# Performance work log

Hardware: AMD Instinct MI355X
Metric: run time of the kernel (lower is better)

Reference implementation:

```python
import jax, jax.numpy as jnp
import numpy as np

N_EMBD = 64
HEAD_SIZE = 64
BLOCK_SIZE = 256

def setup_inputs() -> dict:
    key = jax.random.key(0)
    ks = jax.random.split(key, 7)
    B, T, C = 2048, 256, N_EMBD
    scale = 1.0 / np.sqrt(C)
    inputs = jax.random.normal(ks[0], (B, T, C), dtype=jnp.float32)
    Wk = jax.random.uniform(ks[1], (C, HEAD_SIZE), jnp.float32, -scale, scale)
    bk = jax.random.uniform(ks[2], (HEAD_SIZE,), jnp.float32, -scale, scale)
    Wq = jax.random.uniform(ks[3], (C, HEAD_SIZE), jnp.float32, -scale, scale)
    bq = jax.random.uniform(ks[4], (HEAD_SIZE,), jnp.float32, -scale, scale)
    Wv = jax.random.uniform(ks[5], (C, HEAD_SIZE), jnp.float32, -scale, scale)
    bv = jax.random.uniform(ks[6], (HEAD_SIZE,), jnp.float32, -scale, scale)
    return {"inputs": inputs, "Wk": Wk, "bk": bk, "Wq": Wq, "bq": bq, "Wv": Wv, "bv": bv}

def reference(inputs, Wk, bk, Wq, bq, Wv, bv):
    T = inputs.shape[1]
    k = inputs @ Wk + bk          # [B,T,H]
    q = inputs @ Wq + bq          # [B,T,H]
    v = inputs @ Wv + bv          # [B,T,H]
    scores = jnp.einsum('bqh,bkh->bqk', q, k) / jnp.sqrt(jnp.asarray(k.shape[-1], k.dtype))
    causal = jnp.tril(jnp.ones((T, T), dtype=bool))
    scores = jnp.where(causal, scores, -jnp.inf)
    attn = jax.nn.softmax(scores, axis=-1)
    return jnp.einsum('bqk,bkh->bqh', attn, v)
```

## Files before the change

kernel.cpp:

```cpp
#include <hip/hip_runtime.h>

typedef short s8v __attribute__((ext_vector_type(8)));
typedef short s4v __attribute__((ext_vector_type(4)));
typedef float f4v __attribute__((ext_vector_type(4)));
typedef unsigned int u32;

#define MFMA16(a,b,c) __builtin_amdgcn_mfma_f32_16x16x32_bf16((a),(b),(c),0,0,0)

__device__ __forceinline__ unsigned short f2bf(float x) {
  union { float f; unsigned u; } v; v.f = x;
  unsigned r = v.u + 0x7FFFu + ((v.u >> 16) & 1u);
  return (unsigned short)(r >> 16);
}

__device__ __forceinline__ u32 cvtpk(float lo, float hi) {
  u32 r;
  asm("v_cvt_pk_bf16_f32 %0, %1, %2" : "=v"(r) : "v"(lo), "v"(hi));
  return r;
}

__global__ void prep_wt(const float* __restrict__ Wk, const float* __restrict__ Wq,
                        const float* __restrict__ Wv, unsigned short* __restrict__ WT) {
  int i = blockIdx.x * 256 + threadIdx.x;
  if (i >= 64 * 64) return;
  int n = i >> 6, k = i & 63;
  WT[i]            = f2bf(Wk[k * 64 + n]);
  WT[4096 + i]     = f2bf(Wq[k * 64 + n] * (0.125f * 1.44269504f));
  WT[2 * 4096 + i] = f2bf(Wv[k * 64 + n]);
}

__global__ __launch_bounds__(512, 4) void head_fused(
    const float* __restrict__ X, const unsigned short* __restrict__ WT,
    const float* __restrict__ bk, const float* __restrict__ bq,
    const float* __restrict__ bv, float* __restrict__ Out)
{
  __shared__ char lds[65536];
  char* Kl = lds;
  char* Vt = lds + 32768;
  const int tid  = threadIdx.x;
  const int wave = tid >> 6;
  const int lane = tid & 63;
  const int lrow = lane & 15;
  const int lgrp = lane >> 4;

  const float* Xb = X + (size_t)blockIdx.x * (256 * 64);
  float* Ob = Out + (size_t)blockIdx.x * (256 * 64);

  auto xfrag = [&](int tt, int kk) -> s8v {
    const float* p = Xb + (tt * 16 + lrow) * 64 + kk * 32 + lgrp * 8;
    f4v a = *(const f4v*)p;
    f4v b = *(const f4v*)(p + 4);
    union { u32 u[4]; s8v v; } r;
    r.u[0] = cvtpk(a[0], a[1]); r.u[1] = cvtpk(a[2], a[3]);
    r.u[2] = cvtpk(b[0], b[1]); r.u[3] = cvtpk(b[2], b[3]);
    return r.v;
  };

  s8v qf[2][2];
  {
    float biasq[4];
#pragma unroll
    for (int nt = 0; nt < 4; ++nt) biasq[nt] = bq[nt * 16 + lrow] * (0.125f * 1.44269504f);
    s8v wfQ[4][2];
#pragma unroll
    for (int nt = 0; nt < 4; ++nt)
#pragma unroll
      for (int kk = 0; kk < 2; ++kk)
        wfQ[nt][kk] = *(const s8v*)(WT + 4096 + (nt * 16 + lrow) * 64 + kk * 32 + lgrp * 8);
#pragma unroll
    for (int i = 0; i < 2; ++i) {
      const int t = i ? (15 - wave) : wave;
      char* scw = Kl + wave * 4096 + i * 2048;
      const s8v x0 = xfrag(t, 0);
      const s8v x1 = xfrag(t, 1);
#pragma unroll
      for (int nt = 0; nt < 4; ++nt) {
        f4v a = {0.f, 0.f, 0.f, 0.f};
        a = MFMA16(x0, wfQ[nt][0], a);
        a = MFMA16(x1, wfQ[nt][1], a);
        const u32 c01 = cvtpk(a[0] + biasq[nt], a[1] + biasq[nt]);
        const u32 c23 = cvtpk(a[2] + biasq[nt], a[3] + biasq[nt]);
        const int col2 = (nt * 16 + lrow) * 2;
#pragma unroll
        for (int r = 0; r < 4; ++r) {
          const int row = lgrp * 4 + r;
          const int off = (row * 128 + col2) ^ ((row & 7) << 4);
          const u32 w = (r < 2) ? c01 : c23;
          *(unsigned short*)(scw + off) = (unsigned short)((r & 1) ? (w >> 16) : (w & 0xffff));
        }
      }
    }
    asm volatile("s_waitcnt lgkmcnt(0)" ::: "memory");
    __builtin_amdgcn_sched_barrier(0);
#pragma unroll
    for (int i = 0; i < 2; ++i) {
      char* scw = Kl + wave * 4096 + i * 2048;
      qf[i][0] = *(const s8v*)(scw + ((lrow * 128 + lgrp * 16) ^ ((lrow & 7) << 4)));
      qf[i][1] = *(const s8v*)(scw + ((lrow * 128 + 64 + lgrp * 16) ^ ((lrow & 7) << 4)));
    }
    asm volatile("s_waitcnt lgkmcnt(0)" ::: "memory");
    __builtin_amdgcn_sched_barrier(0);
  }

  {
    float biask[4], biasv[4];
#pragma unroll
    for (int nt = 0; nt < 4; ++nt) {
      biask[nt] = bk[nt * 16 + lrow];
      biasv[nt] = bv[nt * 16 + lrow];
    }
#pragma unroll
    for (int it = 0; it < 2; ++it) {
      const int tt = wave * 2 + it;
      const s8v x0 = xfrag(tt, 0);
      const s8v x1 = xfrag(tt, 1);
#pragma unroll
      for (int nt = 0; nt < 4; ++nt) {
        const s8v wk0 = *(const s8v*)(WT + (nt * 16 + lrow) * 64 + lgrp * 8);
        const s8v wk1 = *(const s8v*)(WT + (nt * 16 + lrow) * 64 + 32 + lgrp * 8);
        const s8v wv0 = *(const s8v*)(WT + 2 * 4096 + (nt * 16 + lrow) * 64 + lgrp * 8);
        const s8v wv1 = *(const s8v*)(WT + 2 * 4096 + (nt * 16 + lrow) * 64 + 32 + lgrp * 8);
        f4v aK = {0.f, 0.f, 0.f, 0.f};
        aK = MFMA16(x0, wk0, aK);
        aK = MFMA16(x1, wk1, aK);
        const u32 k01 = cvtpk(aK[0] + biask[nt], aK[1] + biask[nt]);
        const u32 k23 = cvtpk(aK[2] + biask[nt], aK[3] + biask[nt]);
        const int col2 = (nt * 16 + lrow) * 2;
#pragma unroll
        for (int r = 0; r < 4; ++r) {
          const int row = tt * 16 + lgrp * 4 + r;
          const int off = (row * 128 + col2) ^ ((row & 7) << 4);
          const u32 w = (r < 2) ? k01 : k23;
          *(unsigned short*)(Kl + off) = (unsigned short)((r & 1) ? (w >> 16) : (w & 0xffff));
        }
        f4v aV = {0.f, 0.f, 0.f, 0.f};
        aV = MFMA16(x0, wv0, aV);
        aV = MFMA16(x1, wv1, aV);
        const int h = nt * 16 + lrow;
        union { u32 u[2]; s4v v; } pk;
        pk.u[0] = cvtpk(aV[0] + biasv[nt], aV[1] + biasv[nt]);
        pk.u[1] = cvtpk(aV[2] + biasv[nt], aV[3] + biasv[nt]);
        const int tp = (tt >> 1) * 32 + 8 * lgrp + 4 * (tt & 1);
        const int offv = (h * 512 + tp * 2) ^ ((h & 7) << 4);
        *(s4v*)(Vt + offv) = pk.v;
      }
    }
  }

  __syncthreads();

#pragma unroll
  for (int i = 0; i < 2; ++i) {
    const int t = i ? (15 - wave) : wave;
    const int nblk = (t >> 1) + 1;
    const int qrow = t * 16 + lrow;
    f4v Oa[4];
#pragma unroll
    for (int nt = 0; nt < 4; ++nt) Oa[nt] = (f4v){0.f, 0.f, 0.f, 0.f};
    float ll = 0.f;

    for (int b2 = 0; b2 < nblk; ++b2) {
      const int rb = b2 * 32;
      const s8v kf0a = *(const s8v*)(Kl + (((rb + lrow) * 128 + lgrp * 16) ^ ((lrow & 7) << 4)));
      const s8v kf0b = *(const s8v*)(Kl + (((rb + lrow) * 128 + 64 + lgrp * 16) ^ ((lrow & 7) << 4)));
      const s8v kf1a = *(const s8v*)(Kl + (((rb + 16 + lrow) * 128 + lgrp * 16) ^ ((lrow & 7) << 4)));
      const s8v kf1b = *(const s8v*)(Kl + (((rb + 16 + lrow) * 128 + 64 + lgrp * 16) ^ ((lrow & 7) << 4)));

      f4v S0 = {0.f,0.f,0.f,0.f}, S1 = {0.f,0.f,0.f,0.f};
      __builtin_amdgcn_s_setprio(1);
      S0 = MFMA16(kf0a, qf[i][0], S0);
      S0 = MFMA16(kf0b, qf[i][1], S0);
      S1 = MFMA16(kf1a, qf[i][0], S1);
      S1 = MFMA16(kf1b, qf[i][1], S1);
      __builtin_amdgcn_s_setprio(0);

      if (b2 == nblk - 1) {
#pragma unroll
        for (int r = 0; r < 4; ++r) {
          const int k0 = rb + lgrp * 4 + r;
          if (k0 > qrow)      S0[r] = -1e30f;
          if (k0 + 16 > qrow) S1[r] = -1e30f;
        }
      }

#pragma unroll
      for (int r = 0; r < 4; ++r) {
        S0[r] = __builtin_amdgcn_exp2f(fminf(S0[r], 30.f));
        S1[r] = __builtin_amdgcn_exp2f(fminf(S1[r], 30.f));
      }
      ll += ((S0[0] + S0[1]) + (S0[2] + S0[3])) + ((S1[0] + S1[1]) + (S1[2] + S1[3]));

      union { u32 u[4]; s8v v; } pu;
      pu.u[0] = cvtpk(S0[0], S0[1]);
      pu.u[1] = cvtpk(S0[2], S0[3]);
      pu.u[2] = cvtpk(S1[0], S1[1]);
      pu.u[3] = cvtpk(S1[2], S1[3]);

      s8v vf[4];
#pragma unroll
      for (int nt = 0; nt < 4; ++nt)
        vf[nt] = *(const s8v*)(Vt + (((nt * 16 + lrow) * 512 + b2 * 64 + lgrp * 16) ^ ((lrow & 7) << 4)));

      __builtin_amdgcn_s_setprio(1);
#pragma unroll
      for (int nt = 0; nt < 4; ++nt) Oa[nt] = MFMA16(vf[nt], pu.v, Oa[nt]);
      __builtin_amdgcn_s_setprio(0);
    }

    float lls = ll + __shfl_xor(ll, 16);
    lls += __shfl_xor(lls, 32);
    const float inv = 1.0f / lls;
#pragma unroll
    for (int nt = 0; nt < 4; ++nt) {
      f4v o;
#pragma unroll
      for (int r = 0; r < 4; ++r) o[r] = Oa[nt][r] * inv;
      *(f4v*)(Ob + (size_t)qrow * 64 + nt * 16 + lgrp * 4) = o;
    }
  }
}

extern "C" void kernel_launch(void* const* d_in, const int* in_sizes, int n_in,
                              void* d_out, int out_size, void* d_ws, size_t ws_size,
                              hipStream_t stream) {
  const float* X  = (const float*)d_in[0];
  const float* Wk = (const float*)d_in[1];
  const float* bk = (const float*)d_in[2];
  const float* Wq = (const float*)d_in[3];
  const float* bq = (const float*)d_in[4];
  const float* Wv = (const float*)d_in[5];
  const float* bv = (const float*)d_in[6];
  float* Out = (float*)d_out;
  unsigned short* WT = (unsigned short*)d_ws;

  const int B = in_sizes[0] / (256 * 64);
  prep_wt<<<dim3(16), dim3(256), 0, stream>>>(Wk, Wq, Wv, WT);
  head_fused<<<dim3(B), dim3(512), 0, stream>>>(X, WT, bk, bq, bv, Out);
}
```

Baseline: 130.5 us.

## Double block to 16 waves and split attention key blocks across wave pairs

The fused head kernel now launches 1024 threads (16 waves) per batch instead of 512. Each wave projects one 16-row tile of Q/K/V, and wave pairs share two query tiles, each wave taking alternating key blocks. Partial outputs and row sums are combined through LDS after extra barriers. The intent is more waves to hide latency and better balance of the causal work, at the cost of more synchronisation, a larger LDS footprint (68 KB, which may limit blocks per CU), and a tighter register budget from launch bounds (1024, 8).

```diff
diff --git a/kernel.cpp b/kernel.cpp
--- a/kernel.cpp
+++ b/kernel.cpp
@@ -29,12 +29,12 @@
   WT[2 * 4096 + i] = f2bf(Wv[k * 64 + n]);
 }
 
-__global__ __launch_bounds__(512, 4) void head_fused(
+__global__ __launch_bounds__(1024, 8) void head_fused(
     const float* __restrict__ X, const unsigned short* __restrict__ WT,
     const float* __restrict__ bk, const float* __restrict__ bq,
     const float* __restrict__ bv, float* __restrict__ Out)
 {
-  __shared__ char lds[65536];
+  __shared__ char lds[69632];
   char* Kl = lds;
   char* Vt = lds + 32768;
   const int tid  = threadIdx.x;
@@ -42,12 +42,15 @@
   const int lane = tid & 63;
   const int lrow = lane & 15;
   const int lgrp = lane >> 4;
+  const int pair = wave >> 1;
+  const int sub  = wave & 1;
+  const int t0 = pair, t1 = 15 - pair;
 
   const float* Xb = X + (size_t)blockIdx.x * (256 * 64);
   float* Ob = Out + (size_t)blockIdx.x * (256 * 64);
 
-  auto xfrag = [&](int tt, int kk) -> s8v {
-    const float* p = Xb + (tt * 16 + lrow) * 64 + kk * 32 + lgrp * 8;
+  auto xfrag = [&](int kk) -> s8v {
+    const float* p = Xb + (wave * 16 + lrow) * 64 + kk * 32 + lgrp * 8;
     f4v a = *(const f4v*)p;
     f4v b = *(const f4v*)(p + 4);
     union { u32 u[4]; s8v v; } r;
@@ -55,52 +58,45 @@
     r.u[2] = cvtpk(b[0], b[1]); r.u[3] = cvtpk(b[2], b[3]);
     return r.v;
   };
-
-  s8v qf[2][2];
+  const s8v x0 = xfrag(0);
+  const s8v x1 = xfrag(1);
+
   {
     float biasq[4];
 #pragma unroll
     for (int nt = 0; nt < 4; ++nt) biasq[nt] = bq[nt * 16 + lrow] * (0.125f * 1.44269504f);
-    s8v wfQ[4][2];
-#pragma unroll
-    for (int nt = 0; nt < 4; ++nt)
-#pragma unroll
-      for (int kk = 0; kk < 2; ++kk)
-        wfQ[nt][kk] = *(const s8v*)(WT + 4096 + (nt * 16 + lrow) * 64 + kk * 32 + lgrp * 8);
-#pragma unroll
-    for (int i = 0; i < 2; ++i) {
-      const int t = i ? (15 - wave) : wave;
-      char* scw = Kl + wave * 4096 + i * 2048;
-      const s8v x0 = xfrag(t, 0);
-      const s8v x1 = xfrag(t, 1);
-#pragma unroll
-      for (int nt = 0; nt < 4; ++nt) {
-        f4v a = {0.f, 0.f, 0.f, 0.f};
-        a = MFMA16(x0, wfQ[nt][0], a);
-        a = MFMA16(x1, wfQ[nt][1], a);
-        const u32 c01 = cvtpk(a[0] + biasq[nt], a[1] + biasq[nt]);
-        const u32 c23 = cvtpk(a[2] + biasq[nt], a[3] + biasq[nt]);
-        const int col2 = (nt * 16 + lrow) * 2;
-#pragma unroll
-        for (int r = 0; r < 4; ++r) {
-          const int row = lgrp * 4 + r;
-          const int off = (row * 128 + col2) ^ ((row & 7) << 4);
-          const u32 w = (r < 2) ? c01 : c23;
-          *(unsigned short*)(scw + off) = (unsigned short)((r & 1) ? (w >> 16) : (w & 0xffff));
-        }
+    char* scw = Kl + wave * 2048;
+#pragma unroll
+    for (int nt = 0; nt < 4; ++nt) {
+      const s8v wq0 = *(const s8v*)(WT + 4096 + (nt * 16 + lrow) * 64 + lgrp * 8);
+      const s8v wq1 = *(const s8v*)(WT + 4096 + (nt * 16 + lrow) * 64 + 32 + lgrp * 8);
+      f4v a = {0.f, 0.f, 0.f, 0.f};
+      a = MFMA16(x0, wq0, a);
+      a = MFMA16(x1, wq1, a);
+      const u32 c01 = cvtpk(a[0] + biasq[nt], a[1] + biasq[nt]);
+      const u32 c23 = cvtpk(a[2] + biasq[nt], a[3] + biasq[nt]);
+      const int col2 = (nt * 16 + lrow) * 2;
+#pragma unroll
+      for (int r = 0; r < 4; ++r) {
+        const int row = lgrp * 4 + r;
+        const int off = (row * 128 + col2) ^ ((row & 7) << 4);
+        const u32 w = (r < 2) ? c01 : c23;
+        *(unsigned short*)(scw + off) = (unsigned short)((r & 1) ? (w >> 16) : (w & 0xffff));
       }
     }
-    asm volatile("s_waitcnt lgkmcnt(0)" ::: "memory");
-    __builtin_amdgcn_sched_barrier(0);
-#pragma unroll
-    for (int i = 0; i < 2; ++i) {
-      char* scw = Kl + wave * 4096 + i * 2048;
-      qf[i][0] = *(const s8v*)(scw + ((lrow * 128 + lgrp * 16) ^ ((lrow & 7) << 4)));
-      qf[i][1] = *(const s8v*)(scw + ((lrow * 128 + 64 + lgrp * 16) ^ ((lrow & 7) << 4)));
-    }
-    asm volatile("s_waitcnt lgkmcnt(0)" ::: "memory");
-    __builtin_amdgcn_sched_barrier(0);
-  }
+  }
+  __syncthreads();
+
+  s8v qf0[2], qf1[2];
+  {
+    char* s0 = Kl + t0 * 2048;
+    char* s1 = Kl + t1 * 2048;
+    qf0[0] = *(const s8v*)(s0 + ((lrow * 128 + lgrp * 16) ^ ((lrow & 7) << 4)));
+    qf0[1] = *(const s8v*)(s0 + ((lrow * 128 + 64 + lgrp * 16) ^ ((lrow & 7) << 4)));
+    qf1[0] = *(const s8v*)(s1 + ((lrow * 128 + lgrp * 16) ^ ((lrow & 7) << 4)));
+    qf1[1] = *(const s8v*)(s1 + ((lrow * 128 + 64 + lgrp * 16) ^ ((lrow & 7) << 4)));
+  }
+  __syncthreads();
 
   {
     float biask[4], biasv[4];
@@ -109,112 +105,153 @@
       biask[nt] = bk[nt * 16 + lrow];
       biasv[nt] = bv[nt * 16 + lrow];
     }
-#pragma unroll
-    for (int it = 0; it < 2; ++it) {
-      const int tt = wave * 2 + it;
-      const s8v x0 = xfrag(tt, 0);
-      const s8v x1 = xfrag(tt, 1);
-#pragma unroll
-      for (int nt = 0; nt < 4; ++nt) {
-        const s8v wk0 = *(const s8v*)(WT + (nt * 16 + lrow) * 64 + lgrp * 8);
-        const s8v wk1 = *(const s8v*)(WT + (nt * 16 + lrow) * 64 + 32 + lgrp * 8);
-        const s8v wv0 = *(const s8v*)(WT + 2 * 4096 + (nt * 16 + lrow) * 64 + lgrp * 8);
-        const s8v wv1 = *(const s8v*)(WT + 2 * 4096 + (nt * 16 + lrow) * 64 + 32 + lgrp * 8);
-        f4v aK = {0.f, 0.f, 0.f, 0.f};
-        aK = MFMA16(x0, wk0, aK);
-        aK = MFMA16(x1, wk1, aK);
-        const u32 k01 = cvtpk(aK[0] + biask[nt], aK[1] + biask[nt]);
-        const u32 k23 = cvtpk(aK[2] + biask[nt], aK[3] + biask[nt]);
-        const int col2 = (nt * 16 + lrow) * 2;
-#pragma unroll
-        for (int r = 0; r < 4; ++r) {
-          const int row = tt * 16 + lgrp * 4 + r;
-          const int off = (row * 128 + col2) ^ ((row & 7) << 4);
-          const u32 w = (r < 2) ? k01 : k23;
-          *(unsigned short*)(Kl + off) = (unsigned short)((r & 1) ? (w >> 16) : (w & 0xffff));
-        }
-        f4v aV = {0.f, 0.f, 0.f, 0.f};
-        aV = MFMA16(x0, wv0, aV);
-        aV = MFMA16(x1, wv1, aV);
-        const int h = nt * 16 + lrow;
-        union { u32 u[2]; s4v v; } pk;
-        pk.u[0] = cvtpk(aV[0] + biasv[nt], aV[1] + biasv[nt]);
-        pk.u[1] = cvtpk(aV[2] + biasv[nt], aV[3] + biasv[nt]);
-        const int tp = (tt >> 1) * 32 + 8 * lgrp + 4 * (tt & 1);
-        const int offv = (h * 512 + tp * 2) ^ ((h & 7) << 4);
-        *(s4v*)(Vt + offv) = pk.v;
+    const int tt = wave;
+#pragma unroll
+    for (int nt = 0; nt < 4; ++nt) {
+      const s8v wk0 = *(const s8v*)(WT + (nt * 16 + lrow) * 64 + lgrp * 8);
+      const s8v wk1 = *(const s8v*)(WT + (nt * 16 + lrow) * 64 + 32 + lgrp * 8);
+      const s8v wv0 = *(const s8v*)(WT + 2 * 4096 + (nt * 16 + lrow) * 64 + lgrp * 8);
+      const s8v wv1 = *(const s8v*)(WT + 2 * 4096 + (nt * 16 + lrow) * 64 + 32 + lgrp * 8);
+      f4v aK = {0.f, 0.f, 0.f, 0.f};
+      aK = MFMA16(x0, wk0, aK);
+      aK = MFMA16(x1, wk1, aK);
+      const u32 k01 = cvtpk(aK[0] + biask[nt], aK[1] + biask[nt]);
+      const u32 k23 = cvtpk(aK[2] + biask[nt], aK[3] + biask[nt]);
+      const int col2 = (nt * 16 + lrow) * 2;
+#pragma unroll
+      for (int r = 0; r < 4; ++r) {
+        const int row = tt * 16 + lgrp * 4 + r;
+        const int off = (row * 128 + col2) ^ ((row & 7) << 4);
+        const u32 w = (r < 2) ? k01 : k23;
+        *(unsigned short*)(Kl + off) = (unsigned short)((r & 1) ? (w >> 16) : (w & 0xffff));
       }
-    }
-  }
-
-  __syncthreads();
-
-#pragma unroll
-  for (int i = 0; i < 2; ++i) {
-    const int t = i ? (15 - wave) : wave;
-    const int nblk = (t >> 1) + 1;
+      f4v aV = {0.f, 0.f, 0.f, 0.f};
+      aV = MFMA16(x0, wv0, aV);
+      aV = MFMA16(x1, wv1, aV);
+      const int h = nt * 16 + lrow;
+      union { u32 u[2]; s4v v; } pk;
+      pk.u[0] = cvtpk(aV[0] + biasv[nt], aV[1] + biasv[nt]);
+      pk.u[1] = cvtpk(aV[2] + biasv[nt], aV[3] + biasv[nt]);
+      const int tp = (tt >> 1) * 32 + 8 * lgrp + 4 * (tt & 1);
+      const int offv = (h * 512 + tp * 2) ^ ((h & 7) << 4);
+      *(s4v*)(Vt + offv) = pk.v;
+    }
+  }
+  __syncthreads();
+
+  f4v Oa0[4], Oa1[4];
+  float ll0 = 0.f, ll1 = 0.f;
+#pragma unroll
+  for (int nt = 0; nt < 4; ++nt) {
+    Oa0[nt] = (f4v){0.f, 0.f, 0.f, 0.f};
+    Oa1[nt] = (f4v){0.f, 0.f, 0.f, 0.f};
+  }
+
+  auto proc = [&](int t, int b2, const s8v* qf, f4v* Oa, float& ll) {
+    const int rb = b2 * 32;
     const int qrow = t * 16 + lrow;
-    f4v Oa[4];
-#pragma unroll
-    for (int nt = 0; nt < 4; ++nt) Oa[nt] = (f4v){0.f, 0.f, 0.f, 0.f};
-    float ll = 0.f;
-
-    for (int b2 = 0; b2 < nblk; ++b2) {
-      const int rb = b2 * 32;
-      const s8v kf0a = *(const s8v*)(Kl + (((rb + lrow) * 128 + lgrp * 16) ^ ((lrow & 7) << 4)));
-      const s8v kf0b = *(const s8v*)(Kl + (((rb + lrow) * 128 + 64 + lgrp * 16) ^ ((lrow & 7) << 4)));
-      const s8v kf1a = *(const s8v*)(Kl + (((rb + 16 + lrow) * 128 + lgrp * 16) ^ ((lrow & 7) << 4)));
-      const s8v kf1b = *(const s8v*)(Kl + (((rb + 16 + lrow) * 128 + 64 + lgrp * 16) ^ ((lrow & 7) << 4)));
-
-      f4v S0 = {0.f,0.f,0.f,0.f}, S1 = {0.f,0.f,0.f,0.f};
-      __builtin_amdgcn_s_setprio(1);
-      S0 = MFMA16(kf0a, qf[i][0], S0);
-      S0 = MFMA16(kf0b, qf[i][1], S0);
-      S1 = MFMA16(kf1a, qf[i][0], S1);
-      S1 = MFMA16(kf1b, qf[i][1], S1);
-      __builtin_amdgcn_s_setprio(0);
-
-      if (b2 == nblk - 1) {
-#pragma unroll
-        for (int r = 0; r < 4; ++r) {
-          const int k0 = rb + lgrp * 4 + r;
-          if (k0 > qrow)      S0[r] = -1e30f;
-          if (k0 + 16 > qrow) S1[r] = -1e30f;
-        }
+    const s8v kf0a = *(const s8v*)(Kl + (((rb + lrow) * 128 + lgrp * 16) ^ ((lrow & 7) << 4)));
+    const s8v kf0b = *(const s8v*)(Kl + (((rb + lrow) * 128 + 64 + lgrp * 16) ^ ((lrow & 7) << 4)));
+    const s8v kf1a = *(const s8v*)(Kl + (((rb + 16 + lrow) * 128 + lgrp * 16) ^ ((lrow & 7) << 4)));
+    const s8v kf1b = *(const s8v*)(Kl + (((rb + 16 + lrow) * 128 + 64 + lgrp * 16) ^ ((lrow & 7) << 4)));
+
+    f4v S0 = {0.f,0.f,0.f,0.f}, S1 = {0.f,0.f,0.f,0.f};
+    __builtin_amdgcn_s_setprio(1);
+    S0 = MFMA16(kf0a, qf[0], S0);
+    S0 = MFMA16(kf0b, qf[1], S0);
+    S1 = MFMA16(kf1a, qf[0], S1);
+    S1 = MFMA16(kf1b, qf[1], S1);
+    __builtin_amdgcn_s_setprio(0);
+
+    if (b2 == (t >> 1)) {
+#pragma unroll
+      for (int r = 0; r < 4; ++r) {
+        const int k0 = rb + lgrp * 4 + r;
+        if (k0 > qrow)      S0[r] = -1e30f;
+        if (k0 + 16 > qrow) S1[r] = -1e30f;
       }
-
-#pragma unroll
-      for (int r = 0; r < 4; ++r) {
-        S0[r] = __builtin_amdgcn_exp2f(fminf(S0[r], 30.f));
-        S1[r] = __builtin_amdgcn_exp2f(fminf(S1[r], 30.f));
-      }
-      ll += ((S0[0] + S0[1]) + (S0[2] + S0[3])) + ((S1[0] + S1[1]) + (S1[2] + S1[3]));
-
-      union { u32 u[4]; s8v v; } pu;
-      pu.u[0] = cvtpk(S0[0], S0[1]);
-      pu.u[1] = cvtpk(S0[2], S0[3]);
-      pu.u[2] = cvtpk(S1[0], S1[1]);
-      pu.u[3] = cvtpk(S1[2], S1[3]);
-
-      s8v vf[4];
-#pragma unroll
-      for (int nt = 0; nt < 4; ++nt)
-        vf[nt] = *(const s8v*)(Vt + (((nt * 16 + lrow) * 512 + b2 * 64 + lgrp * 16) ^ ((lrow & 7) << 4)));
-
-      __builtin_amdgcn_s_setprio(1);
-#pragma unroll
-      for (int nt = 0; nt < 4; ++nt) Oa[nt] = MFMA16(vf[nt], pu.v, Oa[nt]);
-      __builtin_amdgcn_s_setprio(0);
-    }
-
-    float lls = ll + __shfl_xor(ll, 16);
+    }
+
+#pragma unroll
+    for (int r = 0; r < 4; ++r) {
+      S0[r] = __builtin_amdgcn_exp2f(fminf(S0[r], 30.f));
+      S1[r] = __builtin_amdgcn_exp2f(fminf(S1[r], 30.f));
+    }
+    ll += ((S0[0] + S0[1]) + (S0[2] + S0[3])) + ((S1[0] + S1[1]) + (S1[2] + S1[3]));
+
+    union { u32 u[4]; s8v v; } pu;
+    pu.u[0] = cvtpk(S0[0], S0[1]);
+    pu.u[1] = cvtpk(S0[2], S0[3]);
+    pu.u[2] = cvtpk(S1[0], S1[1]);
+    pu.u[3] = cvtpk(S1[2], S1[3]);
+
+    s8v vf[4];
+#pragma unroll
+    for (int nt = 0; nt < 4; ++nt)
+      vf[nt] = *(const s8v*)(Vt + (((nt * 16 + lrow) * 512 + b2 * 64 + lgrp * 16) ^ ((lrow & 7) << 4)));
+
+    __builtin_amdgcn_s_setprio(1);
+#pragma unroll
+    for (int nt = 0; nt < 4; ++nt) Oa[nt] = MFMA16(vf[nt], pu.v, Oa[nt]);
+    __builtin_amdgcn_s_setprio(0);
+  };
+
+  const int nb1 = (t1 >> 1) + 1;
+  const int nb0 = (t0 >> 1) + 1;
+  for (int b2 = sub; b2 < nb1; b2 += 2) proc(t1, b2, qf1, Oa1, ll1);
+  for (int b2 = sub; b2 < nb0; b2 += 2) proc(t0, b2, qf0, Oa0, ll0);
+
+  __syncthreads();
+
+  char* slot0 = lds +         pair * 4352 + lane * 68;
+  char* slot1 = lds + 34816 + pair * 4352 + lane * 68;
+  if (sub) {
+#pragma unroll
+    for (int nt = 0; nt < 4; ++nt)
+#pragma unroll
+      for (int r = 0; r < 4; ++r) *(float*)(slot0 + (nt * 4 + r) * 4) = Oa0[nt][r];
+    *(float*)(slot0 + 64) = ll0;
+  } else {
+#pragma unroll
+    for (int nt = 0; nt < 4; ++nt)
+#pragma unroll
+      for (int r = 0; r < 4; ++r) *(float*)(slot1 + (nt * 4 + r) * 4) = Oa1[nt][r];
+    *(float*)(slot1 + 64) = ll1;
+  }
+  __syncthreads();
+
+  if (!sub) {
+#pragma unroll
+    for (int nt = 0; nt < 4; ++nt)
+#pragma unroll
+      for (int r = 0; r < 4; ++r) Oa0[nt][r] += *(float*)(slot0 + (nt * 4 + r) * 4);
+    ll0 += *(float*)(slot0 + 64);
+    float lls = ll0 + __shfl_xor(ll0, 16);
     lls += __shfl_xor(lls, 32);
     const float inv = 1.0f / lls;
+    const int qrow = t0 * 16 + lrow;
 #pragma unroll
     for (int nt = 0; nt < 4; ++nt) {
       f4v o;
 #pragma unroll
-      for (int r = 0; r < 4; ++r) o[r] = Oa[nt][r] * inv;
+      for (int r = 0; r < 4; ++r) o[r] = Oa0[nt][r] * inv;
+      *(f4v*)(Ob + (size_t)qrow * 64 + nt * 16 + lgrp * 4) = o;
+    }
+  } else {
+#pragma unroll
+    for (int nt = 0; nt < 4; ++nt)
+#pragma unroll
+      for (int r = 0; r < 4; ++r) Oa1[nt][r] += *(float*)(slot1 + (nt * 4 + r) * 4);
+    ll1 += *(float*)(slot1 + 64);
+    float lls = ll1 + __shfl_xor(ll1, 16);
+    lls += __shfl_xor(lls, 32);
+    const float inv = 1.0f / lls;
+    const int qrow = t1 * 16 + lrow;
+#pragma unroll
+    for (int nt = 0; nt < 4; ++nt) {
+      f4v o;
+#pragma unroll
+      for (int r = 0; r < 4; ++r) o[r] = Oa1[nt][r] * inv;
       *(f4v*)(Ob + (size_t)qrow * 64 + nt * 16 + lgrp * 4) = o;
     }
   }
@@ -235,5 +272,5 @@
 
   const int B = in_sizes[0] / (256 * 64);
   prep_wt<<<dim3(16), dim3(256), 0, stream>>>(Wk, Wq, Wv, WT);
-  head_fused<<<dim3(B), dim3(512), 0, stream>>>(X, WT, bk, bq, bv, Out);
-}
+  head_fused<<<dim3(B), dim3(1024), 0, stream>>>(X, WT, bk, bq, bv, Out);
+}
```

Measured after the change: 193.5 us. +48.3%, slower.

## Split causal query tiles across twelve waves to balance attention work

Applied to the files above, without the earlier changes.

The block grows from 8 to 12 waves. Waves 0-7 each take one of the large causal query tiles (8-15). Waves 8-11 each take a pair of small tiles, so every wave's key-block count stays at or below the old per-wave load. The K/V projection tiles and the Q scratch areas are redistributed to match, and an extra barrier protects the Q scratch before K/V writes. The launch bound moves to 6 waves per SIMD, which tightens the VGPR budget and may cause spills. The longer inline code for the paired tiles adds its own register pressure.

```diff
diff --git a/kernel.cpp b/kernel.cpp
--- a/kernel.cpp
+++ b/kernel.cpp
@@ -29,7 +29,7 @@
   WT[2 * 4096 + i] = f2bf(Wv[k * 64 + n]);
 }
 
-__global__ __launch_bounds__(512, 4) void head_fused(
+__global__ __launch_bounds__(768, 6) void head_fused(
     const float* __restrict__ X, const unsigned short* __restrict__ WT,
     const float* __restrict__ bk, const float* __restrict__ bq,
     const float* __restrict__ bv, float* __restrict__ Out)
@@ -43,6 +43,9 @@
   const int lrow = lane & 15;
   const int lgrp = lane >> 4;
 
+  const int ta = (wave < 8) ? (15 - wave) : (wave - 8);
+  const int tb = (wave < 8) ? -1 : (15 - wave);
+
   const float* Xb = X + (size_t)blockIdx.x * (256 * 64);
   float* Ob = Out + (size_t)blockIdx.x * (256 * 64);
 
@@ -56,7 +59,7 @@
     return r.v;
   };
 
-  s8v qf[2][2];
+  s8v qfa0, qfa1, qfb0, qfb1;
   {
     float biasq[4];
 #pragma unroll
@@ -67,10 +70,10 @@
 #pragma unroll
       for (int kk = 0; kk < 2; ++kk)
         wfQ[nt][kk] = *(const s8v*)(WT + 4096 + (nt * 16 + lrow) * 64 + kk * 32 + lgrp * 8);
-#pragma unroll
-    for (int i = 0; i < 2; ++i) {
-      const int t = i ? (15 - wave) : wave;
-      char* scw = Kl + wave * 4096 + i * 2048;
+    char* scw0 = Kl + wave * 2048;
+    char* scw1 = Vt + wave * 2048;
+
+    auto qproj = [&](int t, char* scw) {
       const s8v x0 = xfrag(t, 0);
       const s8v x1 = xfrag(t, 1);
 #pragma unroll
@@ -89,18 +92,24 @@
           *(unsigned short*)(scw + off) = (unsigned short)((r & 1) ? (w >> 16) : (w & 0xffff));
         }
       }
-    }
+    };
+    qproj(ta, scw0);
+    if (tb >= 0) qproj(tb, scw1);
+
     asm volatile("s_waitcnt lgkmcnt(0)" ::: "memory");
     __builtin_amdgcn_sched_barrier(0);
-#pragma unroll
-    for (int i = 0; i < 2; ++i) {
-      char* scw = Kl + wave * 4096 + i * 2048;
-      qf[i][0] = *(const s8v*)(scw + ((lrow * 128 + lgrp * 16) ^ ((lrow & 7) << 4)));
-      qf[i][1] = *(const s8v*)(scw + ((lrow * 128 + 64 + lgrp * 16) ^ ((lrow & 7) << 4)));
+    qfa0 = *(const s8v*)(scw0 + ((lrow * 128 + lgrp * 16) ^ ((lrow & 7) << 4)));
+    qfa1 = *(const s8v*)(scw0 + ((lrow * 128 + 64 + lgrp * 16) ^ ((lrow & 7) << 4)));
+    if (tb >= 0) {
+      qfb0 = *(const s8v*)(scw1 + ((lrow * 128 + lgrp * 16) ^ ((lrow & 7) << 4)));
+      qfb1 = *(const s8v*)(scw1 + ((lrow * 128 + 64 + lgrp * 16) ^ ((lrow & 7) << 4)));
+    } else {
+      qfb0 = qfa0; qfb1 = qfa1;
     }
     asm volatile("s_waitcnt lgkmcnt(0)" ::: "memory");
     __builtin_amdgcn_sched_barrier(0);
   }
+  __syncthreads();
 
   {
     float biask[4], biasv[4];
@@ -109,9 +118,9 @@
       biask[nt] = bk[nt * 16 + lrow];
       biasv[nt] = bv[nt * 16 + lrow];
     }
-#pragma unroll
-    for (int it = 0; it < 2; ++it) {
-      const int tt = wave * 2 + it;
+    const int nproj = (wave >= 8) ? 2 : 1;
+    for (int it = 0; it < nproj; ++it) {
+      const int tt = wave + it * 4;
       const s8v x0 = xfrag(tt, 0);
       const s8v x1 = xfrag(tt, 1);
 #pragma unroll
@@ -146,12 +155,9 @@
       }
     }
   }
-
   __syncthreads();
 
-#pragma unroll
-  for (int i = 0; i < 2; ++i) {
-    const int t = i ? (15 - wave) : wave;
+  auto attn = [&](int t, s8v qk0, s8v qk1) {
     const int nblk = (t >> 1) + 1;
     const int qrow = t * 16 + lrow;
     f4v Oa[4];
@@ -168,10 +174,10 @@
 
       f4v S0 = {0.f,0.f,0.f,0.f}, S1 = {0.f,0.f,0.f,0.f};
       __builtin_amdgcn_s_setprio(1);
-      S0 = MFMA16(kf0a, qf[i][0], S0);
-      S0 = MFMA16(kf0b, qf[i][1], S0);
-      S1 = MFMA16(kf1a, qf[i][0], S1);
-      S1 = MFMA16(kf1b, qf[i][1], S1);
+      S0 = MFMA16(kf0a, qk0, S0);
+      S0 = MFMA16(kf0b, qk1, S0);
+      S1 = MFMA16(kf1a, qk0, S1);
+      S1 = MFMA16(kf1b, qk1, S1);
       __builtin_amdgcn_s_setprio(0);
 
       if (b2 == nblk - 1) {
@@ -217,7 +223,10 @@
       for (int r = 0; r < 4; ++r) o[r] = Oa[nt][r] * inv;
       *(f4v*)(Ob + (size_t)qrow * 64 + nt * 16 + lgrp * 4) = o;
     }
-  }
+  };
+
+  attn(ta, qfa0, qfa1);
+  if (tb >= 0) attn(tb, qfb0, qfb1);
 }
 
 extern "C" void kernel_launch(void* const* d_in, const int* in_sizes, int n_in,
@@ -235,5 +244,5 @@
 
   const int B = in_sizes[0] / (256 * 64);
   prep_wt<<<dim3(16), dim3(256), 0, stream>>>(Wk, Wq, Wv, WT);
-  head_fused<<<dim3(B), dim3(512), 0, stream>>>(X, WT, bk, bq, bv, Out);
-}
+  head_fused<<<dim3(B), dim3(768), 0, stream>>>(X, WT, bk, bq, bv, Out);
+}
```

Result: slower. 164.7 us (+26.2%).
